# Performance work log

Hardware: AMD Instinct MI355X
Metric: run time of the kernel (lower is better)

Reference implementation:

```python
import jax, jax.numpy as jnp
import numpy as np

B, S, D, H = 2, 2048, 1024, 16
DK = D // H  # 64
THETA = 10000.0


def setup_inputs() -> dict:
    key = jax.random.key(0)
    ks = jax.random.split(key, 5)
    sigma = (2.0 / (D + DK)) ** 0.5
    return {
        "x": jax.random.normal(ks[0], (B, S, D), jnp.float32),
        "Wq": jax.random.normal(ks[1], (D, H * DK), jnp.float32) * sigma,
        "Wk": jax.random.normal(ks[2], (D, H * DK), jnp.float32) * sigma,
        "Wv": jax.random.normal(ks[3], (D, H * DK), jnp.float32) * sigma,
        "Wo": jax.random.normal(ks[4], (D, H * DK), jnp.float32) * sigma,
        "token_positions": jnp.arange(S, dtype=jnp.int32),
    }


def _rope(x, pos):
    # x: (B, H, S, DK); pos: (S,). Block-diag 2x2 rotation == paired rotation.
    half = DK // 2
    k = jnp.arange(half, dtype=jnp.float32)
    inv_freq = 1.0 / (THETA ** (2.0 * k / DK))          # (half,)
    ang = pos.astype(jnp.float32)[:, None] * inv_freq    # (S, half)
    cos, sin = jnp.cos(ang), jnp.sin(ang)
    xr = x.reshape(*x.shape[:-1], half, 2)
    x0, x1 = xr[..., 0], xr[..., 1]
    o0 = x0 * cos - x1 * sin
    o1 = x0 * sin + x1 * cos
    return jnp.stack([o0, o1], axis=-1).reshape(x.shape)


def reference(x, Wq, Wk, Wv, Wo, token_positions):
    # projections: einsum('... d_in, hd d_in -> ... hd') == x @ W.T
    def proj(W):
        return (x @ W.T).reshape(B, S, H, DK).transpose(0, 2, 1, 3)  # (B,H,S,DK)

    q, k, v = proj(Wq), proj(Wk), proj(Wv)
    q = _rope(q, token_positions)
    k = _rope(k, token_positions)

    scores = jnp.einsum("bhqd,bhkd->bhqk", q, k) / jnp.sqrt(jnp.float32(DK))
    causal = jnp.tril(jnp.ones((S, S), bool))  # (S,S), True where attended
    scores = jnp.where(causal[None, None], scores, -jnp.inf)
    probs = jax.nn.softmax(scores, axis=-1)

    o = jnp.einsum("bhqk,bhkd->bhqd", probs, v)
    o = o.transpose(0, 2, 1, 3).reshape(B, S, H * DK)
    return o @ Wo.T  # einsum('... d_out, d_model d_out -> ... d_model')
```

## Files before the change

### kernel.cpp

```cpp
#include <hip/hip_runtime.h>

typedef __bf16 bf16;
typedef __bf16 bf16x4 __attribute__((ext_vector_type(4)));
typedef __bf16 bf16x8 __attribute__((ext_vector_type(8)));
typedef float f32x4 __attribute__((ext_vector_type(4)));

#define MFMA16(a, b, c) __builtin_amdgcn_mfma_f32_16x16x32_bf16((a), (b), (c), 0, 0, 0)

constexpr int B_ = 2, S_ = 2048, D_ = 1024, H_ = 16, DK_ = 64;

__device__ __forceinline__ void gload16(const bf16* g, bf16* l)
{
  __builtin_amdgcn_global_load_lds(
      (const __attribute__((address_space(1))) uint32_t*)g,
      (__attribute__((address_space(3))) uint32_t*)l, 16, 0, 0);
}

__global__ __launch_bounds__(256) void cvt_k(
    const float* __restrict__ x, const float* __restrict__ Wq, const float* __restrict__ Wk,
    const float* __restrict__ Wv, const float* __restrict__ Wo, bf16* __restrict__ ws)
{
  size_t f = ((size_t)blockIdx.x * 256 + threadIdx.x) * 4;
  const float* src;
  bf16* dst;
  size_t off;
  if (f < 4194304) {
    src = x; dst = ws; off = f;
  } else {
    size_t g = f - 4194304;
    int wsel = (int)(g >> 20);
    off = g & 1048575;
    src = wsel == 0 ? Wq : wsel == 1 ? Wk : wsel == 2 ? Wv : Wo;
    dst = ws + 4194304 + ((size_t)wsel << 20);
  }
  float4 v = *(const float4*)(src + off);
  bf16x4 o = {(bf16)v.x, (bf16)v.y, (bf16)v.z, (bf16)v.w};
  *(bf16x4*)(dst + off) = o;
}

template <typename TY, int PERM>
__global__ __launch_bounds__(256) void gemm_k(
    const bf16* __restrict__ A,
    const bf16* __restrict__ W0, const bf16* __restrict__ W1, const bf16* __restrict__ W2,
    TY* __restrict__ Y0, TY* __restrict__ Y1, TY* __restrict__ Y2,
    int Kdim, float scale0)
{
  __shared__ __align__(16) bf16 As[128 * 64];
  __shared__ __align__(16) bf16 Bs[128 * 64];
  const int t = threadIdx.x, l = t & 63, w = t >> 6;
  const int wm = w >> 1, wn = w & 1;
  const int m0 = blockIdx.x * 128, n0 = blockIdx.y * 128;
  const int z = blockIdx.z;
  const bf16* W = z == 0 ? W0 : z == 1 ? W1 : W2;
  TY* Y = z == 0 ? Y0 : z == 1 ? Y1 : Y2;
  const float scale = (PERM == 1 && z == 0) ? scale0 : 1.0f;

  f32x4 acc[4][4] = {};

  for (int k0 = 0; k0 < Kdim; k0 += 64) {
    __syncthreads();
#pragma unroll
    for (int j = 0; j < 4; ++j) {
      int slot = j * 256 + t;
      int row = slot >> 3, c8 = slot & 7;
      int csw = (c8 ^ (row & 7)) << 3;
      gload16(A + (size_t)(m0 + row) * Kdim + k0 + csw, &As[(j * 256 + w * 64) * 8]);
      gload16(W + (size_t)(n0 + row) * Kdim + k0 + csw, &Bs[(j * 256 + w * 64) * 8]);
    }
    asm volatile("s_waitcnt vmcnt(0)" ::: "memory");
    __syncthreads();
#pragma unroll
    for (int kk = 0; kk < 2; ++kk) {
      bf16x8 af[4], bfr[4];
#pragma unroll
      for (int i = 0; i < 4; ++i) {
        int Ra = wm * 64 + i * 16 + (l & 15);
        int Rb = wn * 64 + i * 16 + (l & 15);
        int c = kk * 4 + (l >> 4);
        af[i] = *(const bf16x8*)&As[Ra * 64 + ((c ^ (Ra & 7)) << 3)];
        bfr[i] = *(const bf16x8*)&Bs[Rb * 64 + ((c ^ (Rb & 7)) << 3)];
      }
#pragma unroll
      for (int mi = 0; mi < 4; ++mi)
#pragma unroll
        for (int ni = 0; ni < 4; ++ni)
          acc[mi][ni] = MFMA16(af[mi], bfr[ni], acc[mi][ni]);
    }
  }

#pragma unroll
  for (int mi = 0; mi < 4; ++mi)
#pragma unroll
    for (int ni = 0; ni < 4; ++ni)
#pragma unroll
      for (int j = 0; j < 4; ++j) {
        int m = m0 + wm * 64 + mi * 16 + (l >> 4) * 4 + j;
        int n = n0 + wn * 64 + ni * 16 + (l & 15);
        float v = acc[mi][ni][j] * scale;
        if (PERM == 0) {
          Y[(size_t)m * 1024 + n] = (TY)v;
        } else {
          int b = m >> 11, s = m & (S_ - 1), h = n >> 6, d = n & (DK_ - 1);
          Y[(((size_t)(b * H_ + h)) * S_ + s) * DK_ + d] = (TY)v;
        }
      }
}

__global__ __launch_bounds__(256) void rope_k(
    bf16* __restrict__ K, const int* __restrict__ pos)
{
  int idx = blockIdx.x * 256 + threadIdx.x;
  int kpg = idx & 3;
  int s = (idx >> 2) & (S_ - 1);
  int bh = idx >> 13;
  float p = (float)pos[s];
  size_t off = ((size_t)bh * S_ + s) * DK_ + kpg * 16;
  bf16x8 lo = *(const bf16x8*)(K + off);
  bf16x8 hi = *(const bf16x8*)(K + off + 8);
  bf16x8 olo, ohi;
#pragma unroll
  for (int ii = 0; ii < 8; ++ii) {
    int kp = kpg * 8 + ii;
    float ang = p * exp2f((float)kp * -0.41524101186017f);
    float sn, cs;
    __sincosf(ang, &sn, &cs);
    float x0 = (float)((ii < 4 ? lo : hi)[(ii & 3) * 2]);
    float x1 = (float)((ii < 4 ? lo : hi)[(ii & 3) * 2 + 1]);
    bf16 o0 = (bf16)(x0 * cs - x1 * sn);
    bf16 o1 = (bf16)(x0 * sn + x1 * cs);
    if (ii < 4) { olo[(ii & 3) * 2] = o0; olo[(ii & 3) * 2 + 1] = o1; }
    else        { ohi[(ii & 3) * 2] = o0; ohi[(ii & 3) * 2 + 1] = o1; }
  }
  *(bf16x8*)(K + off) = olo;
  *(bf16x8*)(K + off + 8) = ohi;
}

__global__ __launch_bounds__(512, 2) void attn_k(
    const bf16* __restrict__ Q, const bf16* __restrict__ K, const bf16* __restrict__ V,
    const int* __restrict__ pos, bf16* __restrict__ O)
{
  __shared__ __align__(16) bf16 Klds[2][64 * 64];
  __shared__ __align__(16) bf16 Vt[2][64 * 64];
  __shared__ __align__(16) bf16 Ps[8][16 * 64];

  const int t = threadIdx.x, l = t & 63, w = t >> 6;
  const int wl = w & 3;
  const int bx = blockIdx.x;
  const int i5 = bx >> 5;
  const int bh = bx & 31;
  const int a = i5 & 7, bq = i5 >> 3;
  const int qt2 = bq ? a : (15 - a);
  const int b = bh >> 4, h = bh & 15;
  const size_t base = (size_t)bh * S_ * DK_;
  const int q0 = qt2 * 128;
  const int ntk = 2 * qt2 + 2;
  const int myqt = 2 * qt2 + (w >> 2);

  const int qrow = w * 16 + (l & 15), qcol = (l >> 4) * 8;
  const bf16* pq = Q + base + (size_t)(q0 + qrow) * 64 + qcol;
  bf16x8 aq0 = *(const bf16x8*)pq, aq1 = *(const bf16x8*)(pq + 32);
  {
    float p = (float)pos[q0 + qrow];
#pragma unroll
    for (int i2 = 0; i2 < 4; ++i2) {
      int kp = (l >> 4) * 4 + i2;
      float s0, c0, s1, c1;
      __sincosf(p * exp2f((float)kp * -0.41524101186017f), &s0, &c0);
      __sincosf(p * exp2f((float)(kp + 16) * -0.41524101186017f), &s1, &c1);
      float x0 = (float)aq0[2 * i2], x1 = (float)aq0[2 * i2 + 1];
      aq0[2 * i2] = (bf16)(x0 * c0 - x1 * s0);
      aq0[2 * i2 + 1] = (bf16)(x0 * s0 + x1 * c0);
      x0 = (float)aq1[2 * i2]; x1 = (float)aq1[2 * i2 + 1];
      aq1[2 * i2] = (bf16)(x0 * c1 - x1 * s1);
      aq1[2 * i2 + 1] = (bf16)(x0 * s1 + x1 * c1);
    }
  }

  {
    int row = t >> 3, c8 = t & 7;
    gload16(K + base + (size_t)row * 64 + ((c8 ^ (row & 7)) << 3),
            &Klds[0][(w * 64) * 8]);
    const bf16* pv = V + base + (size_t)l * 64 + w * 8;
    bf16x8 v0 = *(const bf16x8*)pv;
    asm volatile("s_waitcnt vmcnt(0)" ::: "memory");
#pragma unroll
    for (int ii = 0; ii < 8; ++ii) {
      int d0 = w * 8 + ii;
      Vt[0][d0 * 64 + (((l >> 3) ^ (d0 & 7)) << 3) + (l & 7)] = v0[ii];
    }
  }
  __syncthreads();

  f32x4 acc[4] = {};
  float lsum[4] = {0.f, 0.f, 0.f, 0.f};

  int cur = 0;
  for (int tk = 0; tk < ntk; ++tk) {
    const int nxt = cur ^ 1;
    const bool hasn = (tk + 1) < ntk;
    bf16x8 v0;
    if (hasn) {
      const int kv0n = (tk + 1) * 64;
      int row = t >> 3, c8 = t & 7;
      gload16(K + base + (size_t)(kv0n + row) * 64 + ((c8 ^ (row & 7)) << 3),
              &Klds[nxt][(w * 64) * 8]);
      v0 = *(const bf16x8*)(V + base + (size_t)(kv0n + l) * 64 + w * 8);
    }

    if (tk <= myqt) {
      f32x4 sc[4];
      __builtin_amdgcn_s_setprio(1);
#pragma unroll
      for (int nf = 0; nf < 4; ++nf) {
        int R = nf * 16 + (l & 15);
        int c0 = l >> 4;
        bf16x8 b0 = *(const bf16x8*)&Klds[cur][R * 64 + ((c0 ^ (R & 7)) << 3)];
        bf16x8 b1 = *(const bf16x8*)&Klds[cur][R * 64 + (((4 + c0) ^ (R & 7)) << 3)];
        f32x4 s = {};
        s = MFMA16(aq0, b0, s);
        s = MFMA16(aq1, b1, s);
        sc[nf] = s;
      }
      __builtin_amdgcn_s_setprio(0);

      if (tk == myqt) {
#pragma unroll
        for (int nf = 0; nf < 4; ++nf)
#pragma unroll
          for (int j = 0; j < 4; ++j) {
            int kvl = nf * 16 + (l & 15);
            int ql = wl * 16 + (l >> 4) * 4 + j;
            if (kvl > ql) sc[nf][j] = -1e30f;
          }
      }

#pragma unroll
      for (int nf = 0; nf < 4; ++nf)
#pragma unroll
        for (int j = 0; j < 4; ++j) {
          float p = exp2f(sc[nf][j]);
          lsum[j] += p;
          int r = (l >> 4) * 4 + j, c = nf * 16 + (l & 15);
          Ps[w][r * 64 + ((((c >> 3) ^ (r & 7))) << 3) + (c & 7)] = (bf16)p;
        }

      asm volatile("s_waitcnt lgkmcnt(0)" ::: "memory");

      __builtin_amdgcn_s_setprio(1);
#pragma unroll
      for (int kk = 0; kk < 2; ++kk) {
        int rp = l & 15;
        int c8p = kk * 4 + (l >> 4);
        bf16x8 ap = *(const bf16x8*)&Ps[w][rp * 64 + ((c8p ^ (rp & 7)) << 3)];
#pragma unroll
        for (int nf = 0; nf < 4; ++nf) {
          int R = nf * 16 + (l & 15);
          bf16x8 bv = *(const bf16x8*)&Vt[cur][R * 64 + ((c8p ^ (R & 7)) << 3)];
          acc[nf] = MFMA16(ap, bv, acc[nf]);
        }
      }
      __builtin_amdgcn_s_setprio(0);
    }

    if (hasn) {
#pragma unroll
      for (int ii = 0; ii < 8; ++ii) {
        int d0 = w * 8 + ii;
        Vt[nxt][d0 * 64 + (((l >> 3) ^ (d0 & 7)) << 3) + (l & 7)] = v0[ii];
      }
      asm volatile("s_waitcnt vmcnt(0)" ::: "memory");
    }
    __syncthreads();
    cur = nxt;
  }

#pragma unroll
  for (int m = 1; m <= 8; m <<= 1)
#pragma unroll
    for (int j = 0; j < 4; ++j)
      lsum[j] += __shfl_xor(lsum[j], m, 64);

#pragma unroll
  for (int nf = 0; nf < 4; ++nf)
#pragma unroll
    for (int j = 0; j < 4; ++j) {
      int r = w * 16 + (l >> 4) * 4 + j;
      int d = nf * 16 + (l & 15);
      O[((size_t)(b * S_ + q0 + r) * H_ + h) * DK_ + d] = (bf16)(acc[nf][j] / lsum[j]);
    }
}

extern "C" void kernel_launch(void* const* d_in, const int* in_sizes, int n_in,
                              void* d_out, int out_size, void* d_ws, size_t ws_size,
                              hipStream_t stream)
{
  const float* x = (const float*)d_in[0];
  const float* Wq = (const float*)d_in[1];
  const float* Wk = (const float*)d_in[2];
  const float* Wv = (const float*)d_in[3];
  const float* Wo = (const float*)d_in[4];
  const int* pos = (const int*)d_in[5];

  bf16* ws = (bf16*)d_ws;
  const size_t NE = (size_t)B_ * H_ * S_ * DK_;
  bf16* xb = ws;
  bf16* Wqb = ws + NE;
  bf16* Wkb = Wqb + 1048576;
  bf16* Wvb = Wkb + 1048576;
  bf16* Wob = Wvb + 1048576;
  bf16* Qb = Wob + 1048576;
  bf16* Kb = Qb + NE;
  bf16* Vb = Kb + NE;
  bf16* Ob = xb;

  dim3 blk(256);

  hipLaunchKernelGGL(cvt_k, dim3(8192), blk, 0, stream, x, Wq, Wk, Wv, Wo, ws);

  hipLaunchKernelGGL((gemm_k<bf16, 1>), dim3(32, 8, 3), blk, 0, stream,
                     xb, Wqb, Wkb, Wvb, Qb, Kb, Vb, 1024, 0.125f * 1.4426950408889634f);

  hipLaunchKernelGGL(rope_k, dim3(1024), blk, 0, stream, Kb, pos);

  hipLaunchKernelGGL(attn_k, dim3(512), dim3(512), 0, stream, Qb, Kb, Vb, pos, Ob);

  hipLaunchKernelGGL((gemm_k<float, 0>), dim3(32, 8, 1), blk, 0, stream,
                     Ob, Wob, Wob, Wob, (float*)d_out, (float*)d_out, (float*)d_out,
                     1024, 1.0f);
}
```

Before: 129.6 us.

## Software-pipeline QK^T of next KV tile with softmax and PV of current

Restructures the attention loop so the QK^T MFMAs for tile tk+1 are issued between the exp/P-store and the PV MFMAs of tile tk. K tiles are now prefetched two iterations ahead into the double-buffered LDS, and the score registers carry across iterations. This lets matrix work overlap the exponentials and the LDS round trip for P. In exchange it needs more registers to hold the live scores, adds a prologue with an extra barrier, and makes buffer-index reasoning harder.

Result: no change. 131.1 us (+1.2%).

```diff
diff --git a/kernel.cpp b/kernel.cpp
--- a/kernel.cpp
+++ b/kernel.cpp
@@ -178,8 +178,9 @@
 
   {
     int row = t >> 3, c8 = t & 7;
-    gload16(K + base + (size_t)row * 64 + ((c8 ^ (row & 7)) << 3),
-            &Klds[0][(w * 64) * 8]);
+    int csw = (c8 ^ (row & 7)) << 3;
+    gload16(K + base + (size_t)row * 64 + csw, &Klds[0][(w * 64) * 8]);
+    gload16(K + base + (size_t)(64 + row) * 64 + csw, &Klds[1][(w * 64) * 8]);
     const bf16* pv = V + base + (size_t)l * 64 + w * 8;
     bf16x8 v0 = *(const bf16x8*)pv;
     asm volatile("s_waitcnt vmcnt(0)" ::: "memory");
@@ -193,36 +194,37 @@
 
   f32x4 acc[4] = {};
   float lsum[4] = {0.f, 0.f, 0.f, 0.f};
-
-  int cur = 0;
+  f32x4 sc[4];
+
+  __builtin_amdgcn_s_setprio(1);
+#pragma unroll
+  for (int nf = 0; nf < 4; ++nf) {
+    int R = nf * 16 + (l & 15);
+    int c0 = l >> 4;
+    bf16x8 b0 = *(const bf16x8*)&Klds[0][R * 64 + ((c0 ^ (R & 7)) << 3)];
+    bf16x8 b1 = *(const bf16x8*)&Klds[0][R * 64 + (((4 + c0) ^ (R & 7)) << 3)];
+    f32x4 s = {};
+    s = MFMA16(aq0, b0, s);
+    s = MFMA16(aq1, b1, s);
+    sc[nf] = s;
+  }
+  __builtin_amdgcn_s_setprio(0);
+  __syncthreads();
+
   for (int tk = 0; tk < ntk; ++tk) {
-    const int nxt = cur ^ 1;
     const bool hasn = (tk + 1) < ntk;
     bf16x8 v0;
-    if (hasn) {
-      const int kv0n = (tk + 1) * 64;
+    if ((tk + 2) < ntk) {
       int row = t >> 3, c8 = t & 7;
-      gload16(K + base + (size_t)(kv0n + row) * 64 + ((c8 ^ (row & 7)) << 3),
-              &Klds[nxt][(w * 64) * 8]);
-      v0 = *(const bf16x8*)(V + base + (size_t)(kv0n + l) * 64 + w * 8);
-    }
-
-    if (tk <= myqt) {
-      f32x4 sc[4];
-      __builtin_amdgcn_s_setprio(1);
-#pragma unroll
-      for (int nf = 0; nf < 4; ++nf) {
-        int R = nf * 16 + (l & 15);
-        int c0 = l >> 4;
-        bf16x8 b0 = *(const bf16x8*)&Klds[cur][R * 64 + ((c0 ^ (R & 7)) << 3)];
-        bf16x8 b1 = *(const bf16x8*)&Klds[cur][R * 64 + (((4 + c0) ^ (R & 7)) << 3)];
-        f32x4 s = {};
-        s = MFMA16(aq0, b0, s);
-        s = MFMA16(aq1, b1, s);
-        sc[nf] = s;
-      }
-      __builtin_amdgcn_s_setprio(0);
-
+      int csw = (c8 ^ (row & 7)) << 3;
+      gload16(K + base + (size_t)((tk + 2) * 64 + row) * 64 + csw,
+              &Klds[tk & 1][(w * 64) * 8]);
+    }
+    if (hasn)
+      v0 = *(const bf16x8*)(V + base + (size_t)((tk + 1) * 64 + l) * 64 + w * 8);
+
+    const bool act = tk <= myqt;
+    if (act) {
       if (tk == myqt) {
 #pragma unroll
         for (int nf = 0; nf < 4; ++nf)
@@ -233,7 +235,6 @@
             if (kvl > ql) sc[nf][j] = -1e30f;
           }
       }
-
 #pragma unroll
       for (int nf = 0; nf < 4; ++nf)
 #pragma unroll
@@ -243,9 +244,27 @@
           int r = (l >> 4) * 4 + j, c = nf * 16 + (l & 15);
           Ps[w][r * 64 + ((((c >> 3) ^ (r & 7))) << 3) + (c & 7)] = (bf16)p;
         }
-
+    }
+
+    if (hasn && (tk + 1) <= myqt) {
+      __builtin_amdgcn_s_setprio(1);
+#pragma unroll
+      for (int nf = 0; nf < 4; ++nf) {
+        int R = nf * 16 + (l & 15);
+        int c0 = l >> 4;
+        const bf16* Kb = &Klds[(tk + 1) & 1][0];
+        bf16x8 b0 = *(const bf16x8*)&Kb[R * 64 + ((c0 ^ (R & 7)) << 3)];
+        bf16x8 b1 = *(const bf16x8*)&Kb[R * 64 + (((4 + c0) ^ (R & 7)) << 3)];
+        f32x4 s = {};
+        s = MFMA16(aq0, b0, s);
+        s = MFMA16(aq1, b1, s);
+        sc[nf] = s;
+      }
+      __builtin_amdgcn_s_setprio(0);
+    }
+
+    if (act) {
       asm volatile("s_waitcnt lgkmcnt(0)" ::: "memory");
-
       __builtin_amdgcn_s_setprio(1);
 #pragma unroll
       for (int kk = 0; kk < 2; ++kk) {
@@ -255,7 +274,7 @@
 #pragma unroll
         for (int nf = 0; nf < 4; ++nf) {
           int R = nf * 16 + (l & 15);
-          bf16x8 bv = *(const bf16x8*)&Vt[cur][R * 64 + ((c8p ^ (R & 7)) << 3)];
+          bf16x8 bv = *(const bf16x8*)&Vt[tk & 1][R * 64 + ((c8p ^ (R & 7)) << 3)];
           acc[nf] = MFMA16(ap, bv, acc[nf]);
         }
       }
@@ -266,12 +285,11 @@
 #pragma unroll
       for (int ii = 0; ii < 8; ++ii) {
         int d0 = w * 8 + ii;
-        Vt[nxt][d0 * 64 + (((l >> 3) ^ (d0 & 7)) << 3) + (l & 7)] = v0[ii];
+        Vt[(tk + 1) & 1][d0 * 64 + (((l >> 3) ^ (d0 & 7)) << 3) + (l & 7)] = v0[ii];
       }
       asm volatile("s_waitcnt vmcnt(0)" ::: "memory");
     }
     __syncthreads();
-    cur = nxt;
   }
 
 #pragma unroll
```
